# Performance work log

Hardware: AMD Instinct MI355X
Metric: run time of the kernel (lower is better)

The kernel has to match this reference:

```python
import jax, jax.numpy as jnp
import numpy as np
from jax import lax

B, H, W, CL, CC, CD, NH, NP = 8, 48, 48, 384, 384, 384, 12, 4
N = H * W
HD = CL // NH
SCALE = HD ** -0.5


def _pool_mat(n, out=7):
    # torch AdaptiveAvgPool2d bin edges: [floor(i*n/out), ceil((i+1)*n/out))
    M = np.zeros((out, n), np.float32)
    for i in range(out):
        s = (i * n) // out
        e = -(-((i + 1) * n) // out)
        M[i, s:e] = 1.0 / (e - s)
    return jnp.asarray(M)


def _resize_mat(out_n, in_n):
    # bilinear, align_corners=False (torch F.interpolate)
    M = np.zeros((out_n, in_n), np.float32)
    scale = in_n / out_n
    for o in range(out_n):
        src = (o + 0.5) * scale - 0.5
        src = min(max(src, 0.0), in_n - 1.0)
        i0 = int(np.floor(src))
        i1 = min(i0 + 1, in_n - 1)
        f = src - i0
        M[o, i0] += 1.0 - f
        M[o, i1] += f
    return jnp.asarray(M)


def _ln_c(x, g, b):
    # LayerNorm over channel dim of NCHW, eps=1e-6
    mu = jnp.mean(x, axis=1, keepdims=True)
    var = jnp.mean((x - mu) ** 2, axis=1, keepdims=True)
    xn = (x - mu) * lax.rsqrt(var + 1e-6)
    return xn * g[None, :, None, None] + b[None, :, None, None]


def _c1(x, w):
    # 1x1 conv, w: (out,in)
    return jnp.einsum('oc,bchw->bohw', w, x)


def _bilerp(feat, grid):
    # feat (G,C,Hs,Ws), grid (G,M,2) xy in [-1,1]; align_corners=False, zero padding
    G, C, Hs, Ws = feat.shape
    x = (grid[..., 0] + 1.0) * 0.5 * Ws - 0.5
    y = (grid[..., 1] + 1.0) * 0.5 * Hs - 0.5
    x0 = jnp.floor(x)
    y0 = jnp.floor(y)
    fx = x - x0
    fy = y - y0
    featf = feat.transpose(0, 2, 3, 1).reshape(G, Hs * Ws, C)
    x0i = x0.astype(jnp.int32)
    y0i = y0.astype(jnp.int32)

    def corner(ix, iy):
        valid = ((ix >= 0) & (ix < Ws) & (iy >= 0) & (iy < Hs)).astype(feat.dtype)
        flat = jnp.clip(iy, 0, Hs - 1) * Ws + jnp.clip(ix, 0, Ws - 1)
        g = jax.vmap(lambda f, i: f[i])(featf, flat)  # (G,M,C)
        return g * valid[..., None]

    v00 = corner(x0i, y0i)
    v01 = corner(x0i + 1, y0i)
    v10 = corner(x0i, y0i + 1)
    v11 = corner(x0i + 1, y0i + 1)
    w00 = ((1 - fx) * (1 - fy))[..., None]
    w01 = (fx * (1 - fy))[..., None]
    w10 = ((1 - fx) * fy)[..., None]
    w11 = (fx * fy)[..., None]
    return v00 * w00 + v01 * w01 + v10 * w10 + v11 * w11  # (G,M,C)


def _forward(local_feat, context_prior, deformable_x, W_q, W_k, W_v, W_pre, ln1_g, ln1_b,
             W_post, dw_w, dw_b, ln2_g, ln2_b, W_lo, b_lo, W_off, b_off,
             attention_biases, W_p, bn_g, bn_b, bn_mean, bn_var):
    q = _c1(local_feat, W_q)  # (B,CL,H,W)

    # context_offset_guide: 1x1 -> GELU -> adaptive pool 7x7 -> LN(C) -> 1x1 to 32 -> resize
    cg = jax.nn.gelu(_c1(context_prior, W_pre), approximate=False)
    Mh, Mw = _pool_mat(H), _pool_mat(W)
    pooled = jnp.einsum('oh,pw,bchw->bcop', Mh, Mw, cg)
    guide = _c1(_ln_c(pooled, ln1_g, ln1_b), W_post)  # (B,32,7,7)
    Uh, Uw = _resize_mat(H, 7), _resize_mat(W, 7)
    guide = jnp.einsum('Oh,Pw,bchw->bcOP', Uh, Uw, guide)  # (B,32,H,W)

    # local_offset_base: dwconv3x3 -> LN(C) -> GELU -> 1x1 to 32
    dw = lax.conv_general_dilated(local_feat, dw_w, (1, 1), [(1, 1), (1, 1)],
                                  dimension_numbers=('NCHW', 'OIHW', 'NCHW'),
                                  feature_group_count=CL) + dw_b[None, :, None, None]
    lo = jax.nn.gelu(_ln_c(dw, ln2_g, ln2_b), approximate=False)
    lo = _c1(lo, W_lo) + b_lo[None, :, None, None]  # (B,32,H,W)

    fused = jnp.concatenate([guide, lo], axis=1)  # (B,64,H,W)
    off = _c1(fused, W_off) + b_off[None, :, None, None]  # (B,NH*NP*2,H,W)
    off = off.transpose(0, 2, 3, 1).reshape(B, H, W, NH, NP, 2)
    offn = off / jnp.asarray([W, H], dtype=off.dtype)

    ry = (jnp.arange(H, dtype=off.dtype) + 0.5) / H
    rx = (jnp.arange(W, dtype=off.dtype) + 0.5) / W
    ref = jnp.stack([jnp.broadcast_to(rx[None, :], (H, W)),
                     jnp.broadcast_to(ry[:, None], (H, W))], axis=-1)  # (H,W,2) xy
    grid = (ref[None, :, :, None, None, :] + offn) * 2.0 - 1.0  # (B,H,W,NH,NP,2)

    gridh = grid.reshape(B, N, NH, NP, 2).transpose(0, 2, 1, 3, 4)  # (B,NH,N,NP,2)
    grid_r = gridh.reshape(B * NH, N * NP, 2)

    k = _c1(context_prior, W_k).reshape(B * NH, HD, H, W)
    v = _c1(deformable_x, W_v).reshape(B * NH, HD, H, W)
    k_s = _bilerp(k, grid_r).reshape(B, NH, N, NP, HD)
    v_s = _bilerp(v, grid_r).reshape(B, NH, N, NP, HD)

    qh = q.reshape(B, NH, HD, N).transpose(0, 1, 3, 2)  # (B,NH,N,HD)
    scores = jnp.einsum('bhnd,bhnpd->bhnp', qh, k_s) * SCALE

    # relative position bias: idx(p1,p2) = |dy|*W + |dx| (first-seen enumeration)
    px = jnp.clip(jnp.round((gridh[..., 0] + 1.0) * 0.5 * W - 0.5), 0, W - 1).astype(jnp.int32)
    py = jnp.clip(jnp.round((gridh[..., 1] + 1.0) * 0.5 * H - 0.5), 0, H - 1).astype(jnp.int32)
    n = jnp.arange(N, dtype=jnp.int32)
    qy = (n // W)[None, None, :, None]
    qx = (n % W)[None, None, :, None]
    bidx = jnp.abs(qy - py) * W + jnp.abs(qx - px)  # (B,NH,N,NP)
    bias = attention_biases[jnp.arange(NH)[None, :, None, None], bidx]

    attn = jax.nn.softmax(scores + bias, axis=-1)
    out = jnp.einsum('bhnp,bhnpd->bhnd', attn, v_s)  # (B,NH,N,HD)
    out = out.transpose(0, 1, 3, 2).reshape(B, CL, H, W)

    y = _c1(out, W_p)
    y = bn_g[None, :, None, None] * (y - bn_mean[None, :, None, None]) * \
        lax.rsqrt(bn_var[None, :, None, None] + 1e-5) + bn_b[None, :, None, None]
    return y


def setup_inputs():
    ks = jax.random.split(jax.random.key(0), 16)
    f32 = jnp.float32
    d = {
        'local_feat': jax.random.normal(ks[0], (B, CL, H, W), f32),
        'context_prior': jax.random.normal(ks[1], (B, CC, H, W), f32),
        'deformable_x': jax.random.normal(ks[2], (B, CD, H, W), f32),
        'W_q': jax.random.normal(ks[3], (CL, CL), f32) * 0.02,
        'W_k': jax.random.normal(ks[4], (CL, CC), f32) * 0.02,
        'W_v': jax.random.normal(ks[5], (CD, CD), f32) * 0.02,
        'W_pre': jax.random.normal(ks[6], (CC, CC), f32) * 0.02,
        'ln1_g': jnp.ones((CC,), f32),
        'ln1_b': jnp.zeros((CC,), f32),
        'W_post': jax.random.normal(ks[7], (32, CC), f32) * 0.02,
        'dw_w': jax.random.normal(ks[8], (CL, 1, 3, 3), f32) * 0.1,
        'dw_b': jnp.zeros((CL,), f32),
        'ln2_g': jnp.ones((CL,), f32),
        'ln2_b': jnp.zeros((CL,), f32),
        'W_lo': jax.random.normal(ks[9], (32, CL), f32) * 0.02,
        'b_lo': jnp.zeros((32,), f32),
        'W_off': jax.random.normal(ks[10], (NH * NP * 2, 64), f32) * 0.01,
        'b_off': jax.random.normal(ks[11], (NH * NP * 2,), f32) * 0.5,
        'attention_biases': jax.random.normal(ks[12], (NH, H * W), f32) * 0.02,
        'W_p': jax.random.normal(ks[13], (CL, CL), f32) * 0.02,
        'bn_g': jnp.ones((CL,), f32),
        'bn_b': jnp.zeros((CL,), f32),
        'bn_mean': jax.random.normal(ks[14], (CL,), f32) * 0.01,
        'bn_var': jax.random.uniform(ks[15], (CL,), f32, 0.5, 1.5),
    }
    return d


def reference(local_feat, context_prior, deformable_x, W_q, W_k, W_v, W_pre, ln1_g, ln1_b,
              W_post, dw_w, dw_b, ln2_g, ln2_b, W_lo, b_lo, W_off, b_off,
              attention_biases, W_p, bn_g, bn_b, bn_mean, bn_var):
    return _forward(local_feat, context_prior, deformable_x, W_q, W_k, W_v, W_pre, ln1_g,
                    ln1_b, W_post, dw_w, dw_b, ln2_g, ln2_b, W_lo, b_lo, W_off, b_off,
                    attention_biases, W_p, bn_g, bn_b, bn_mean, bn_var)
```

## Files before the change

### kernel.cpp

```cpp
#include <hip/hip_runtime.h>
#include <hip/hip_bf16.h>
#include <math.h>

#define B_ 8
#define H_ 48
#define W_ 48
#define N_ 2304
#define C_ 384
#define NH_ 12
#define NP_ 4
#define HD_ 32
#define SCALE_ 0.17677669529663687f

typedef unsigned short ushort;
typedef short bf16x8 __attribute__((ext_vector_type(8)));
typedef float f32x4 __attribute__((ext_vector_type(4)));

__device__ __forceinline__ float b2f(ushort u) {
    union { float f; unsigned i; } x; x.i = ((unsigned)u) << 16; return x.f;
}
__device__ __forceinline__ ushort f2b(float f) {
    __hip_bfloat16 h = __float2bfloat16(f);
    return *(ushort*)&h;
}
__device__ __forceinline__ float geluf(float x) {
    return 0.5f * x * (1.0f + erff(x * 0.70710678118654752440f));
}
__device__ __forceinline__ int iabs(int x) { return x < 0 ? -x : x; }

__device__ __forceinline__ void gl_lds16(const ushort* g, ushort* l) {
    __builtin_amdgcn_global_load_lds(
        (const __attribute__((address_space(1))) unsigned int*)g,
        (__attribute__((address_space(3))) unsigned int*)l, 16, 0, 0);
}

__global__ void probe_kernel(const void* ones_ptr, int* flag) {
    if (threadIdx.x == 0 && blockIdx.x == 0)
        *flag = (*(const unsigned*)ones_ptr == 0x3F803F80u) ? 1 : 0;
}

#define PREP_MAX 24
struct PrepTab {
    const void* src[PREP_MAX];
    void*       dst[PREP_MAX];
    int         n[PREP_MAX];
    int         tobf[PREP_MAX];
};
__global__ __launch_bounds__(256) void prep_kernel(PrepTab tab, int ne, const int* __restrict__ dflag)
{
    const int isbf = *dflag;
    const int e = blockIdx.y;
    if (e >= ne) return;
    const int n = tab.n[e];
    const void* src = tab.src[e];
    if (tab.tobf[e]) {
        ushort* dst = (ushort*)tab.dst[e];
        if (isbf) {
            const ushort* s = (const ushort*)src;
            for (int i = blockIdx.x * 256 + threadIdx.x; i < n; i += gridDim.x * 256)
                dst[i] = s[i];
        } else {
            const float* s = (const float*)src;
            for (int i = blockIdx.x * 256 + threadIdx.x; i < n; i += gridDim.x * 256)
                dst[i] = f2b(s[i]);
        }
    } else {
        float* dst = (float*)tab.dst[e];
        if (isbf) {
            const ushort* s = (const ushort*)src;
            for (int i = blockIdx.x * 256 + threadIdx.x; i < n; i += gridDim.x * 256)
                dst[i] = b2f(s[i]);
        } else {
            const float* s = (const float*)src;
            for (int i = blockIdx.x * 256 + threadIdx.x; i < n; i += gridDim.x * 256)
                dst[i] = s[i];
        }
    }
}

__global__ void dwt_prep_kernel(const float* __restrict__ WdF, float* __restrict__ WdT)
{
    int c = threadIdx.x;
#pragma unroll
    for (int u = 0; u < 9; u++) WdT[u * C_ + c] = WdF[c * 9 + u];
}

struct TPtrs { const void* src[3]; ushort* dst[3]; };
__global__ __launch_bounds__(256) void transpose3_kernel(TPtrs tp, const int* __restrict__ dflag)
{
    const int isbf = *dflag;
    const int which = blockIdx.z >> 3;
    const int b = blockIdx.z & 7;
    const int n0 = blockIdx.x * 64, c0 = blockIdx.y * 32;
    const void* in = tp.src[which];
    ushort* out = tp.dst[which];
    const int t = threadIdx.x;

    __shared__ unsigned tile[64][33];

    if (isbf) {
        {
            const int c = t >> 3, s = t & 7;
            uint4 v = *(const uint4*)((const ushort*)in + ((size_t)b * C_ + c0 + c) * N_ + n0 + s * 8);
            const int nb = s * 8;
            tile[nb + 0][c] = v.x & 0xffff; tile[nb + 1][c] = v.x >> 16;
            tile[nb + 2][c] = v.y & 0xffff; tile[nb + 3][c] = v.y >> 16;
            tile[nb + 4][c] = v.z & 0xffff; tile[nb + 5][c] = v.z >> 16;
            tile[nb + 6][c] = v.w & 0xffff; tile[nb + 7][c] = v.w >> 16;
        }
        __syncthreads();
        {
            const int n = t >> 2, s = t & 3;
            const int cb = s * 8;
            unsigned p0 = tile[n][cb + 0] | (tile[n][cb + 1] << 16);
            unsigned p1 = tile[n][cb + 2] | (tile[n][cb + 3] << 16);
            unsigned p2 = tile[n][cb + 4] | (tile[n][cb + 5] << 16);
            unsigned p3 = tile[n][cb + 6] | (tile[n][cb + 7] << 16);
            uint4 o; o.x = p0; o.y = p1; o.z = p2; o.w = p3;
            *(uint4*)(out + ((size_t)b * N_ + n0 + n) * C_ + c0 + cb) = o;
        }
    } else {
        float* tf = (float*)&tile[0][0];
        const int tx = t & 31, ty = t >> 5;
        for (int sub = 0; sub < 2; sub++) {
            int ns = n0 + sub * 32;
            __syncthreads();
#pragma unroll
            for (int u = 0; u < 4; u++) {
                int c = ty + u * 8;
                tf[c * 33 + tx] = ((const float*)in)[((size_t)b * C_ + c0 + c) * N_ + ns + tx];
            }
            __syncthreads();
#pragma unroll
            for (int u = 0; u < 4; u++) {
                int n = ty + u * 8;
                out[((size_t)b * N_ + ns + n) * C_ + c0 + tx] = f2b(tf[tx * 33 + n]);
            }
        }
    }
}

struct QKV4Ptrs { const ushort* A[4]; const ushort* Bw[4]; void* Y[4]; };
__global__ __launch_bounds__(256, 5) void gemm_qkv4_kernel(QKV4Ptrs qp)
{
    const int which = blockIdx.z >> 3;
    const int b = blockIdx.z & 7;
    const ushort* Ag = qp.A[which];
    const ushort* Bg = qp.Bw[which];

    __shared__ ushort As[2][128 * 32];
    __shared__ ushort Bs[2][128 * 32];
    const int tid = threadIdx.x;
    const int m0 = blockIdx.x * 128;
    const int n0 = blockIdx.y * 128;
    const int lane = tid & 63, wave = tid >> 6;
    const int wr = wave >> 1, wc = wave & 1;
    const int quad = lane >> 4, l15 = lane & 15;

    f32x4 acc[4][4];
#pragma unroll
    for (int i = 0; i < 4; i++)
#pragma unroll
        for (int j = 0; j < 4; j++) acc[i][j] = (f32x4){0.f, 0.f, 0.f, 0.f};

    const size_t abase = (size_t)b * (size_t)N_ * C_;

    auto stage = [&](int p, int kc) {
#pragma unroll
        for (int u = 0; u < 2; u++) {
            int idx = tid + 256 * u;
            int r = idx >> 2, s = idx & 3;
            gl_lds16(Ag + abase + (size_t)(m0 + r) * C_ + kc + 8 * s, &As[p][idx * 8]);
            gl_lds16(Bg + (size_t)(n0 + r) * C_ + kc + 8 * s, &Bs[p][idx * 8]);
        }
    };

    stage(0, 0);

    const int nt = C_ / 32;
    for (int t = 0; t < nt; ++t) {
        if (t + 1 < nt) {
            stage((t + 1) & 1, (t + 1) * 32);
            asm volatile("s_waitcnt vmcnt(4)" ::: "memory");
        } else {
            asm volatile("s_waitcnt vmcnt(0)" ::: "memory");
        }
        __builtin_amdgcn_s_barrier();
        __builtin_amdgcn_sched_barrier(0);
        const int p = t & 1;
        bf16x8 af[4], bfr[4];
#pragma unroll
        for (int i = 0; i < 4; i++)
            af[i]  = *(const bf16x8*)&As[p][(wr * 64 + i * 16 + l15) * 32 + quad * 8];
#pragma unroll
        for (int j = 0; j < 4; j++)
            bfr[j] = *(const bf16x8*)&Bs[p][(wc * 64 + j * 16 + l15) * 32 + quad * 8];
#pragma unroll
        for (int i = 0; i < 4; i++)
#pragma unroll
            for (int j = 0; j < 4; j++)
                acc[i][j] = __builtin_amdgcn_mfma_f32_16x16x32_bf16(af[i], bfr[j], acc[i][j], 0, 0, 0);
        __builtin_amdgcn_s_barrier();
    }

    if (which < 3) {
        ushort* Yg = (ushort*)qp.Y[which];
#pragma unroll
        for (int i = 0; i < 4; i++) {
#pragma unroll
            for (int r = 0; r < 4; r++) {
                int m = m0 + wr * 64 + i * 16 + quad * 4 + r;
#pragma unroll
                for (int j = 0; j < 4; j++) {
                    int nn = n0 + wc * 64 + j * 16 + l15;
                    Yg[abase + (size_t)m * C_ + nn] = f2b(acc[i][j][r]);
                }
            }
        }
    } else {
        float* Yg = (float*)qp.Y[3];
#pragma unroll
        for (int i = 0; i < 4; i++) {
#pragma unroll
            for (int r = 0; r < 4; r++) {
                int m = m0 + wr * 64 + i * 16 + quad * 4 + r;
#pragma unroll
                for (int j = 0; j < 4; j++) {
                    int nn = n0 + wc * 64 + j * 16 + l15;
                    Yg[abase + (size_t)m * C_ + nn] = geluf(acc[i][j][r]);
                }
            }
        }
    }
}

__global__ __launch_bounds__(256) void gemm_final_splitk(
    const ushort* __restrict__ WpB, const ushort* __restrict__ AOut,
    float* __restrict__ PF0, float* __restrict__ PF1)
{
    const int b  = blockIdx.z >> 1;
    const int ks = blockIdx.z & 1;
    const int kc0 = ks * 192;

    __shared__ ushort As[2][128 * 32];
    __shared__ ushort Bs[2][128 * 32];
    const int tid = threadIdx.x;
    const int m0 = blockIdx.x * 128;
    const int n0 = blockIdx.y * 128;
    const int lane = tid & 63, wave = tid >> 6;
    const int wr = wave >> 1, wc = wave & 1;
    const int quad = lane >> 4, l15 = lane & 15;

    f32x4 acc[4][4];
#pragma unroll
    for (int i = 0; i < 4; i++)
#pragma unroll
        for (int j = 0; j < 4; j++) acc[i][j] = (f32x4){0.f, 0.f, 0.f, 0.f};

    const size_t bbase = (size_t)b * (size_t)N_ * C_;

    auto stage = [&](int p, int kc) {
#pragma unroll
        for (int u = 0; u < 2; u++) {
            int idx = tid + 256 * u;
            int r = idx >> 2, s = idx & 3;
            gl_lds16(WpB + (size_t)(m0 + r) * C_ + kc0 + kc + 8 * s, &As[p][idx * 8]);
            gl_lds16(AOut + bbase + (size_t)(n0 + r) * C_ + kc0 + kc + 8 * s, &Bs[p][idx * 8]);
        }
    };

    stage(0, 0);

    const int nt = 6;
    for (int t = 0; t < nt; ++t) {
        if (t + 1 < nt) {
            stage((t + 1) & 1, (t + 1) * 32);
            asm volatile("s_waitcnt vmcnt(4)" ::: "memory");
        } else {
            asm volatile("s_waitcnt vmcnt(0)" ::: "memory");
        }
        __builtin_amdgcn_s_barrier();
        __builtin_amdgcn_sched_barrier(0);
        const int p = t & 1;
        bf16x8 af[4], bfr[4];
#pragma unroll
        for (int i = 0; i < 4; i++)
            af[i]  = *(const bf16x8*)&As[p][(wr * 64 + i * 16 + l15) * 32 + quad * 8];
#pragma unroll
        for (int j = 0; j < 4; j++)
            bfr[j] = *(const bf16x8*)&Bs[p][(wc * 64 + j * 16 + l15) * 32 + quad * 8];
#pragma unroll
        for (int i = 0; i < 4; i++)
#pragma unroll
            for (int j = 0; j < 4; j++)
                acc[i][j] = __builtin_amdgcn_mfma_f32_16x16x32_bf16(af[i], bfr[j], acc[i][j], 0, 0, 0);
        __builtin_amdgcn_s_barrier();
    }

    float* out = (ks == 0 ? PF0 : PF1) + (size_t)b * (size_t)C_ * N_;
#pragma unroll
    for (int i = 0; i < 4; i++) {
#pragma unroll
        for (int r = 0; r < 4; r++) {
            int m = m0 + wr * 64 + i * 16 + quad * 4 + r;
#pragma unroll
            for (int j = 0; j < 4; j++) {
                int nn = n0 + wc * 64 + j * 16 + l15;
                out[(size_t)m * N_ + nn] = acc[i][j][r];
            }
        }
    }
}

__global__ __launch_bounds__(256) void combine_bn_kernel(
    const float* __restrict__ PF0, const float* __restrict__ PF1,
    void* __restrict__ Yg,
    const float* __restrict__ bng, const float* __restrict__ bnb,
    const float* __restrict__ bnm, const float* __restrict__ bnv,
    const int* __restrict__ dflag)
{
    const int isbf = *dflag;
    const size_t nv4 = (size_t)B_ * C_ * N_ / 4;
    for (size_t i = blockIdx.x * 256 + threadIdx.x; i < nv4; i += (size_t)gridDim.x * 256) {
        const size_t e0 = i * 4;
        const int co = (int)((e0 / N_) % C_);
        float sc = bng[co] * rsqrtf(bnv[co] + 1e-5f);
        float sh = bnb[co] - sc * bnm[co];
        f32x4 a = *(const f32x4*)(PF0 + e0);
        f32x4 b = *(const f32x4*)(PF1 + e0);
        f32x4 v;
#pragma unroll
        for (int j = 0; j < 4; j++) v[j] = sc * (a[j] + b[j]) + sh;
        if (isbf) {
            ushort4 o;
            o.x = f2b(v[0]); o.y = f2b(v[1]); o.z = f2b(v[2]); o.w = f2b(v[3]);
            *(ushort4*)((ushort*)Yg + e0) = o;
        } else {
            *(f32x4*)((float*)Yg + e0) = v;
        }
    }
}

__global__ __launch_bounds__(384) void pool_ln_guide_kernel(
    const float* __restrict__ CG, const float* __restrict__ g, const float* __restrict__ bt,
    const ushort* __restrict__ WpostB, float* __restrict__ G7)
{
    const int cell = blockIdx.x % 49, b = blockIdx.x / 49;
    const int i = cell / 7, j = cell % 7, c = threadIdx.x;
    const int sh = (i * H_) / 7, eh = ((i + 1) * H_ + 6) / 7;
    const int sw = (j * W_) / 7, ew = ((j + 1) * W_ + 6) / 7;
    float s = 0.f;
    for (int h = sh; h < eh; h++)
        for (int w = sw; w < ew; w++)
            s += CG[((size_t)b * N_ + h * W_ + w) * C_ + c];
    s *= 1.0f / (float)((eh - sh) * (ew - sw));

    float rs = s, rq = s * s;
#pragma unroll
    for (int m = 1; m <= 32; m <<= 1) {
        rs += __shfl_xor(rs, m);
        rq += __shfl_xor(rq, m);
    }
    __shared__ float ss[6], sq[6], buf[C_];
    __shared__ float psum[12][33];
    int wid = threadIdx.x >> 6;
    if ((threadIdx.x & 63) == 0) { ss[wid] = rs; sq[wid] = rq; }
    __syncthreads();
    if (threadIdx.x == 0) {
        float ts = 0.f, tq = 0.f;
        for (int k = 0; k < 6; k++) { ts += ss[k]; tq += sq[k]; }
        ss[0] = ts; sq[0] = tq;
    }
    __syncthreads();
    float mu = ss[0] / (float)C_;
    float var = sq[0] / (float)C_ - mu * mu;
    float inv = rsqrtf(var + 1e-6f);
    buf[c] = (s - mu) * inv * g[c] + bt[c];
    __syncthreads();

    const int oc = threadIdx.x & 31, seg = threadIdx.x >> 5;
    const uint4* wp = (const uint4*)(WpostB + oc * C_ + seg * 32);
    float part = 0.f;
#pragma unroll
    for (int u = 0; u < 4; u++) {
        uint4 v = wp[u];
        const float* bb = &buf[seg * 32 + u * 8];
        part += b2f((ushort)(v.x & 0xffff)) * bb[0] + b2f((ushort)(v.x >> 16)) * bb[1];
        part += b2f((ushort)(v.y & 0xffff)) * bb[2] + b2f((ushort)(v.y >> 16)) * bb[3];
        part += b2f((ushort)(v.z & 0xffff)) * bb[4] + b2f((ushort)(v.z >> 16)) * bb[5];
        part += b2f((ushort)(v.w & 0xffff)) * bb[6] + b2f((ushort)(v.w >> 16)) * bb[7];
    }
    psum[seg][oc] = part;
    __syncthreads();
    if (threadIdx.x < 32) {
        float acc = 0.f;
#pragma unroll
        for (int k = 0; k < 12; k++) acc += psum[k][threadIdx.x];
        G7[((size_t)b * 49 + cell) * 32 + threadIdx.x] = acc;
    }
}

__global__ __launch_bounds__(384) void wcomb_prep_kernel(
    const ushort* __restrict__ WoffB, const ushort* __restrict__ WloB,
    const float* __restrict__ bloF, const float* __restrict__ boffF,
    ushort* __restrict__ Bext, float* __restrict__ biasp)
{
    const int co = blockIdx.x;
    const int c = threadIdx.x;
    float acc = 0.f;
#pragma unroll 8
    for (int j = 0; j < 32; j++)
        acc += b2f(WoffB[co * 64 + 32 + j]) * b2f(WloB[j * 384 + c]);
    ushort hi = f2b(acc);
    float r = acc - b2f(hi);
    ushort lo = f2b(r);
    Bext[co * 1152 + c] = hi;
    Bext[co * 1152 + 384 + c] = lo;
    Bext[co * 1152 + 768 + c] = hi;
    if (c == 0) {
        float bp = boffF[co];
        for (int j = 0; j < 32; j++)
            bp += b2f(WoffB[co * 64 + 32 + j]) * bloF[j];
        biasp[co] = bp;
    }
}

__global__ void og7_prep_kernel(
    const ushort* __restrict__ WoffB, const float* __restrict__ G7, float* __restrict__ OG7)
{
    const int bc = blockIdx.x;
    const int co = threadIdx.x;
    if (co >= 96) return;
    const float* g = G7 + (size_t)bc * 32;
    float acc = 0.f;
#pragma unroll 8
    for (int c = 0; c < 32; c++)
        acc += b2f(WoffB[co * 64 + c]) * g[c];
    OG7[(size_t)bc * 96 + co] = acc;
}

__global__ __launch_bounds__(512) void dw_ln_gelu_kernel(
    const ushort* __restrict__ LF, const float* __restrict__ WdT, const float* __restrict__ BdF,
    const float* __restrict__ g, const float* __restrict__ bt,
    ushort* __restrict__ AHI, ushort* __restrict__ ALO)
{
    const int wave = threadIdx.x >> 6, lane = threadIdx.x & 63;
    const int m = blockIdx.x * 8 + wave;
    const int b = m / N_, n = m % N_;
    const int h = n / W_, w = n % W_;
    const bool act = lane < 48;
    const int c0 = lane * 8;

    float acc[8];
#pragma unroll
    for (int j = 0; j < 8; j++) acc[j] = 0.f;
    if (act) {
        f32x4 b0 = *(const f32x4*)(BdF + c0);
        f32x4 b1 = *(const f32x4*)(BdF + c0 + 4);
#pragma unroll
        for (int j = 0; j < 4; j++) { acc[j] = b0[j]; acc[4 + j] = b1[j]; }
    }

#pragma unroll
    for (int u = 0; u < 9; u++) {
        const int ky = u / 3, kx = u % 3;
        const int y = h + ky - 1, x = w + kx - 1;
        if (act && y >= 0 && y < H_ && x >= 0 && x < W_) {
            uint4 v = *(const uint4*)(LF + ((size_t)b * N_ + y * W_ + x) * C_ + c0);
            f32x4 wa = *(const f32x4*)(WdT + u * C_ + c0);
            f32x4 wb = *(const f32x4*)(WdT + u * C_ + c0 + 4);
            acc[0] += wa[0] * b2f((ushort)(v.x & 0xffff));
            acc[1] += wa[1] * b2f((ushort)(v.x >> 16));
            acc[2] += wa[2] * b2f((ushort)(v.y & 0xffff));
            acc[3] += wa[3] * b2f((ushort)(v.y >> 16));
            acc[4] += wb[0] * b2f((ushort)(v.z & 0xffff));
            acc[5] += wb[1] * b2f((ushort)(v.z >> 16));
            acc[6] += wb[2] * b2f((ushort)(v.w & 0xffff));
            acc[7] += wb[3] * b2f((ushort)(v.w >> 16));
        }
    }

    float rs = 0.f, rq = 0.f;
#pragma unroll
    for (int j = 0; j < 8; j++) { rs += acc[j]; rq += acc[j] * acc[j]; }
#pragma unroll
    for (int s = 1; s <= 32; s <<= 1) {
        rs += __shfl_xor(rs, s);
        rq += __shfl_xor(rq, s);
    }
    float mu = rs / (float)C_;
    float var = rq / (float)C_ - mu * mu;
    float inv = rsqrtf(var + 1e-6f);

    if (act) {
        f32x4 g0 = *(const f32x4*)(g + c0);
        f32x4 g1 = *(const f32x4*)(g + c0 + 4);
        f32x4 t0 = *(const f32x4*)(bt + c0);
        f32x4 t1 = *(const f32x4*)(bt + c0 + 4);
        float v[8];
#pragma unroll
        for (int j = 0; j < 4; j++) {
            v[j]     = geluf((acc[j]     - mu) * inv * g0[j] + t0[j]);
            v[4 + j] = geluf((acc[4 + j] - mu) * inv * g1[j] + t1[j]);
        }
        uint4 hi, lo;
        ushort hs[8], ls[8];
#pragma unroll
        for (int j = 0; j < 8; j++) {
            hs[j] = f2b(v[j]);
            ls[j] = f2b(v[j] - b2f(hs[j]));
        }
        hi.x = (unsigned)hs[0] | ((unsigned)hs[1] << 16);
        hi.y = (unsigned)hs[2] | ((unsigned)hs[3] << 16);
        hi.z = (unsigned)hs[4] | ((unsigned)hs[5] << 16);
        hi.w = (unsigned)hs[6] | ((unsigned)hs[7] << 16);
        lo.x = (unsigned)ls[0] | ((unsigned)ls[1] << 16);
        lo.y = (unsigned)ls[2] | ((unsigned)ls[3] << 16);
        lo.z = (unsigned)ls[4] | ((unsigned)ls[5] << 16);
        lo.w = (unsigned)ls[6] | ((unsigned)ls[7] << 16);
        size_t idx = (size_t)m * C_ + c0;
        *(uint4*)(AHI + idx) = hi;
        *(uint4*)(ALO + idx) = lo;
    }
}

__global__ __launch_bounds__(256) void off_gemm_kernel(
    const ushort* __restrict__ AHI, const ushort* __restrict__ ALO,
    const ushort* __restrict__ Bext, float* __restrict__ OFFP)
{
    __shared__ ushort As[4][128 * 32];
    __shared__ ushort Bs[4][128 * 32];
    const int tid = threadIdx.x;
    const int m0 = blockIdx.x * 128;
    const int seg = blockIdx.y;
    const ushort* Ag = (seg < 2) ? AHI : ALO;
    const int bcol0 = seg * 384;
    const int lane = tid & 63, wave = tid >> 6;
    const int wr = wave >> 1, wc = wave & 1;
    const int quad = lane >> 4, l15 = lane & 15;

    f32x4 acc[4][3];
#pragma unroll
    for (int i = 0; i < 4; i++)
#pragma unroll
        for (int j = 0; j < 3; j++) acc[i][j] = (f32x4){0.f, 0.f, 0.f, 0.f};

    auto stage = [&](int p, int kc) {
#pragma unroll
        for (int u = 0; u < 2; u++) {
            int idx = tid + 256 * u;
            int r = idx >> 2, s = idx & 3;
            int rb = r < 96 ? r : 95;
            gl_lds16(Ag + (size_t)(m0 + r) * 384 + kc + 8 * s, &As[p][idx * 8]);
            gl_lds16(Bext + (size_t)rb * 1152 + bcol0 + kc + 8 * s, &Bs[p][idx * 8]);
        }
    };

    stage(0, 0);
    stage(1, 32);
    stage(2, 64);

    const int nt = 12;
    for (int t = 0; t < nt; ++t) {
        if (t + 2 < nt)      asm volatile("s_waitcnt vmcnt(8)" ::: "memory");
        else if (t + 1 < nt) asm volatile("s_waitcnt vmcnt(4)" ::: "memory");
        else                 asm volatile("s_waitcnt vmcnt(0)" ::: "memory");
        __builtin_amdgcn_s_barrier();
        __builtin_amdgcn_sched_barrier(0);
        if (t + 3 < nt) stage((t + 3) & 3, (t + 3) * 32);
        const int p = t & 3;
        bf16x8 af[4], bfr[3];
#pragma unroll
        for (int i = 0; i < 4; i++)
            af[i]  = *(const bf16x8*)&As[p][(wr * 64 + i * 16 + l15) * 32 + quad * 8];
#pragma unroll
        for (int j = 0; j < 3; j++)
            bfr[j] = *(const bf16x8*)&Bs[p][(wc * 48 + j * 16 + l15) * 32 + quad * 8];
#pragma unroll
        for (int i = 0; i < 4; i++)
#pragma unroll
            for (int j = 0; j < 3; j++)
                acc[i][j] = __builtin_amdgcn_mfma_f32_16x16x32_bf16(af[i], bfr[j], acc[i][j], 0, 0, 0);
    }

    float* out = OFFP + (size_t)seg * ((size_t)B_ * N_ * 96);
#pragma unroll
    for (int i = 0; i < 4; i++) {
#pragma unroll
        for (int r = 0; r < 4; r++) {
            int m = m0 + wr * 64 + i * 16 + quad * 4 + r;
#pragma unroll
            for (int j = 0; j < 3; j++) {
                int co = wc * 48 + j * 16 + l15;
                out[(size_t)m * 96 + co] = acc[i][j][r];
            }
        }
    }
}

__global__ __launch_bounds__(384) void attn_kernel(
    const ushort* __restrict__ Q, const ushort* __restrict__ K, const ushort* __restrict__ V,
    const float* __restrict__ OFFP, const float* __restrict__ biasp,
    const float* __restrict__ OG7,
    const float* __restrict__ ABf, ushort* __restrict__ OUT)
{
    const int pairi = blockIdx.x;
    const int b = pairi / (N_ / 2);
    const int n0 = (pairi % (N_ / 2)) * 2;
    const int tid = threadIdx.x;

    __shared__ int   cidxS[96][4];
    __shared__ float cwS[96][4];
    __shared__ float biasS[96];

    if (tid < 96) {
        const int pos = tid / 48, idx = tid % 48;
        const int n = n0 + pos;
        const int h = n / W_, w = n % W_;
        const int nh = idx >> 2, p = idx & 3;
        const int co = nh * 8 + 2 * p;

        const float fs = 7.0f / 48.0f;
        float sy = fminf(fmaxf(((float)h + 0.5f) * fs - 0.5f, 0.f), 6.f);
        float sx = fminf(fmaxf(((float)w + 0.5f) * fs - 0.5f, 0.f), 6.f);
        int gy0 = (int)floorf(sy), gx0 = (int)floorf(sx);
        int gy1 = min(gy0 + 1, 6), gx1 = min(gx0 + 1, 6);
        float gfy = sy - (float)gy0, gfx = sx - (float)gx0;
        float bw00 = (1.f - gfy) * (1.f - gfx), bw01 = (1.f - gfy) * gfx;
        float bw10 = gfy * (1.f - gfx), bw11 = gfy * gfx;
        const float* ogb = OG7 + (size_t)b * 49 * 96;
        int c00 = (gy0 * 7 + gx0) * 96, c01 = (gy0 * 7 + gx1) * 96;
        int c10 = (gy1 * 7 + gx0) * 96, c11 = (gy1 * 7 + gx1) * 96;
        const size_t MS = (size_t)B_ * N_ * 96;
        const size_t mrow = ((size_t)b * N_ + n) * 96;

        float ox = OFFP[mrow + co] + OFFP[MS + mrow + co] + OFFP[2 * MS + mrow + co]
                 + biasp[co]
                 + bw00 * ogb[c00 + co] + bw01 * ogb[c01 + co]
                 + bw10 * ogb[c10 + co] + bw11 * ogb[c11 + co];
        float oy = OFFP[mrow + co + 1] + OFFP[MS + mrow + co + 1] + OFFP[2 * MS + mrow + co + 1]
                 + biasp[co + 1]
                 + bw00 * ogb[c00 + co + 1] + bw01 * ogb[c01 + co + 1]
                 + bw10 * ogb[c10 + co + 1] + bw11 * ogb[c11 + co + 1];

        float x = (float)w + ox;
        float y = (float)h + oy;

        int px = (int)fminf(fmaxf(rintf(x), 0.f), (float)(W_ - 1));
        int py = (int)fminf(fmaxf(rintf(y), 0.f), (float)(H_ - 1));
        biasS[tid] = ABf[(size_t)nh * N_ + iabs(h - py) * W_ + iabs(w - px)];

        float x0f = floorf(x), y0f = floorf(y);
        float fx = x - x0f, fy = y - y0f;
        int x0 = (int)x0f, y0 = (int)y0f;
#pragma unroll
        for (int cc = 0; cc < 4; cc++) {
            int dx = cc & 1, dy = cc >> 1;
            int ix = x0 + dx, iy = y0 + dy;
            bool valid = (ix >= 0) && (ix < W_) && (iy >= 0) && (iy < H_);
            int ixc = min(max(ix, 0), W_ - 1), iyc = min(max(iy, 0), H_ - 1);
            cidxS[tid][cc] = iyc * W_ + ixc;
            float wx = dx ? fx : (1.f - fx);
            float wy = dy ? fy : (1.f - fy);
            cwS[tid][cc] = valid ? wx * wy : 0.f;
        }
    }
    __syncthreads();

    const int pos = tid / 192, r = tid % 192;
    const int nh = r >> 4, dd = r & 15;
    const int n = n0 + pos;
    const size_t row = ((size_t)b * N_ + n) * C_ + nh * HD_ + dd * 2;
    unsigned qu = *(const unsigned*)(Q + row);
    const float q0 = b2f((ushort)(qu & 0xffff));
    const float q1 = b2f((ushort)(qu >> 16));
    const size_t kvbase = (size_t)b * N_ * C_ + nh * HD_ + dd * 2;
    const int s0 = pos * 48 + nh * 4;

    int   ci[NP_][4];
    float cw[NP_][4];
#pragma unroll
    for (int p = 0; p < NP_; p++)
#pragma unroll
        for (int cc = 0; cc < 4; cc++) {
            ci[p][cc] = cidxS[s0 + p][cc];
            cw[p][cc] = cwS[s0 + p][cc];
        }

    float sc[NP_];
#pragma unroll
    for (int p = 0; p < NP_; p++) {
        float ks0 = 0.f, ks1 = 0.f;
#pragma unroll
        for (int cc = 0; cc < 4; cc++) {
            unsigned kv = *(const unsigned*)(K + kvbase + (size_t)ci[p][cc] * C_);
            ks0 += cw[p][cc] * b2f((ushort)(kv & 0xffff));
            ks1 += cw[p][cc] * b2f((ushort)(kv >> 16));
        }
        float dot = q0 * ks0 + q1 * ks1;
#pragma unroll
        for (int m = 1; m <= 8; m <<= 1) dot += __shfl_xor(dot, m);
        sc[p] = dot * SCALE_ + biasS[s0 + p];
    }

    float m = fmaxf(fmaxf(sc[0], sc[1]), fmaxf(sc[2], sc[3]));
    float e[NP_], esum = 0.f;
#pragma unroll
    for (int p = 0; p < NP_; p++) { e[p] = __expf(sc[p] - m); esum += e[p]; }
    float inv = 1.0f / esum;

    float o0 = 0.f, o1 = 0.f;
#pragma unroll
    for (int p = 0; p < NP_; p++) {
        float vs0 = 0.f, vs1 = 0.f;
#pragma unroll
        for (int cc = 0; cc < 4; cc++) {
            unsigned vv = *(const unsigned*)(V + kvbase + (size_t)ci[p][cc] * C_);
            vs0 += cw[p][cc] * b2f((ushort)(vv & 0xffff));
            vs1 += cw[p][cc] * b2f((ushort)(vv >> 16));
        }
        float ep = e[p] * inv;
        o0 += ep * vs0;
        o1 += ep * vs1;
    }
    unsigned ou = (unsigned)f2b(o0) | ((unsigned)f2b(o1) << 16);
    *(unsigned*)(OUT + row) = ou;
}

extern "C" void kernel_launch(void* const* d_in, const int* in_sizes, int n_in,
                              void* d_out, int out_size, void* d_ws, size_t ws_size,
                              hipStream_t stream)
{
    const void* local_feat    = d_in[0];
    const void* context_prior = d_in[1];
    const void* deformable_x  = d_in[2];

    const size_t BIGE = (size_t)B_ * N_ * C_;

    char* wsb = (char*)d_ws;
    auto carve = [&](size_t bytes) { char* p = wsb; wsb += (bytes + 255) & ~(size_t)255; return p; };
    int*    flag = (int*)carve(256);
    ushort* T1   = (ushort*)carve(BIGE * 2);
    ushort* T2   = (ushort*)carve(BIGE * 2);
    ushort* T3   = (ushort*)carve(BIGE * 2);
    ushort* Qb   = (ushort*)carve(BIGE * 2);
    ushort* Kb   = (ushort*)carve(BIGE * 2);
    ushort* Vb   = (ushort*)carve(BIGE * 2);
    ushort* AHI  = (ushort*)carve(BIGE * 2);
    ushort* ALO  = (ushort*)carve(BIGE * 2);
    float*  CGR  = (float*)carve(BIGE * 4);
    float*  OFFB = (float*)carve((size_t)B_ * N_ * 96 * 4 * 3);
    float*  G7   = (float*)carve((size_t)B_ * 49 * 32 * 4);
    ushort* WqB   = (ushort*)carve(147456 * 2);
    ushort* WkB   = (ushort*)carve(147456 * 2);
    ushort* WvB   = (ushort*)carve(147456 * 2);
    ushort* WpreB = (ushort*)carve(147456 * 2);
    ushort* WpB   = (ushort*)carve(147456 * 2);
    ushort* WpostB= (ushort*)carve(12288 * 2);
    ushort* WloB  = (ushort*)carve(12288 * 2);
    ushort* WoffB = (ushort*)carve(6144 * 2);
    ushort* Bext  = (ushort*)carve(96 * 1152 * 2);
    float*  biasp = (float*)carve(96 * 4);
    float*  OG7   = (float*)carve((size_t)B_ * 49 * 96 * 4);
    float*  dwwF  = (float*)carve(3456 * 4);
    float*  dwwT  = (float*)carve(3456 * 4);
    float*  ABf   = (float*)carve(27648 * 4);
    float*  bloF  = (float*)carve(32 * 4);
    float*  boffF = (float*)carve(96 * 4);
    float*  dwbF  = (float*)carve(384 * 4);
    float*  ln1gF = (float*)carve(384 * 4);
    float*  ln1bF = (float*)carve(384 * 4);
    float*  ln2gF = (float*)carve(384 * 4);
    float*  ln2bF = (float*)carve(384 * 4);
    float*  bngF  = (float*)carve(384 * 4);
    float*  bnbF  = (float*)carve(384 * 4);
    float*  bnmF  = (float*)carve(384 * 4);
    float*  bnvF  = (float*)carve(384 * 4);
    ushort* AOut = (ushort*)CGR + BIGE;
    float*  PF0  = (float*)T1;
    float*  PF1  = (float*)T3;

    probe_kernel<<<1, 64, 0, stream>>>(d_in[7] , flag);

    PrepTab tab;
    int ne = 0;
    auto add = [&](const void* s, void* d, int n, int tb) {
        tab.src[ne] = s; tab.dst[ne] = d; tab.n[ne] = n; tab.tobf[ne] = tb; ne++;
    };
    add(d_in[3],  WqB,   147456, 1);
    add(d_in[4],  WkB,   147456, 1);
    add(d_in[5],  WvB,   147456, 1);
    add(d_in[6],  WpreB, 147456, 1);
    add(d_in[19], WpB,   147456, 1);
    add(d_in[9],  WpostB, 12288, 1);
    add(d_in[14], WloB,   12288, 1);
    add(d_in[16], WoffB,   6144, 1);
    add(d_in[10], dwwF,    3456, 0);
    add(d_in[18], ABf,    27648, 0);
    add(d_in[15], bloF,      32, 0);
    add(d_in[17], boffF,     96, 0);
    add(d_in[11], dwbF,     384, 0);
    add(d_in[7],  ln1gF,    384, 0);
    add(d_in[8],  ln1bF,    384, 0);
    add(d_in[12], ln2gF,    384, 0);
    add(d_in[13], ln2bF,    384, 0);
    add(d_in[20], bngF,     384, 0);
    add(d_in[21], bnbF,     384, 0);
    add(d_in[22], bnmF,     384, 0);
    add(d_in[23], bnvF,     384, 0);
    prep_kernel<<<dim3(64, ne), 256, 0, stream>>>(tab, ne, flag);
    dwt_prep_kernel<<<1, 384, 0, stream>>>(dwwF, dwwT);

    dim3 blk256(256);
    dim3 t3grid(N_ / 64, C_ / 32, 3 * B_);
    dim3 qkv4grid(N_ / 128, C_ / 128, 4 * B_);
    dim3 offgrid((B_ * N_) / 128, 3);
    dim3 fingrid(C_ / 128, N_ / 128, 2 * B_);

    TPtrs tp;
    tp.src[0] = local_feat;    tp.dst[0] = T1;
    tp.src[1] = context_prior; tp.dst[1] = T2;
    tp.src[2] = deformable_x;  tp.dst[2] = T3;
    transpose3_kernel<<<t3grid, blk256, 0, stream>>>(tp, flag);

    wcomb_prep_kernel<<<96, 384, 0, stream>>>(WoffB, WloB, bloF, boffF, Bext, biasp);

    dw_ln_gelu_kernel<<<(B_ * N_) / 8, 512, 0, stream>>>(T1, dwwT, dwbF, ln2gF, ln2bF, AHI, ALO);

    off_gemm_kernel<<<offgrid, blk256, 0, stream>>>(AHI, ALO, Bext, OFFB);

    QKV4Ptrs qp;
    qp.A[0] = T1; qp.Bw[0] = WqB;   qp.Y[0] = Qb;
    qp.A[1] = T2; qp.Bw[1] = WkB;   qp.Y[1] = Kb;
    qp.A[2] = T3; qp.Bw[2] = WvB;   qp.Y[2] = Vb;
    qp.A[3] = T2; qp.Bw[3] = WpreB; qp.Y[3] = CGR;
    gemm_qkv4_kernel<<<qkv4grid, blk256, 0, stream>>>(qp);

    pool_ln_guide_kernel<<<B_ * 49, 384, 0, stream>>>(CGR, ln1gF, ln1bF, WpostB, G7);
    og7_prep_kernel<<<B_ * 49, 96, 0, stream>>>(WoffB, G7, OG7);

    attn_kernel<<<(B_ * N_) / 2, 384, 0, stream>>>(Qb, Kb, Vb, OFFB, biasp, OG7, ABf, AOut);

    gemm_final_splitk<<<fingrid, blk256, 0, stream>>>(WpB, AOut, PF0, PF1);

    combine_bn_kernel<<<2048, blk256, 0, stream>>>(PF0, PF1, d_out, bngF, bnbF, bnmF, bnvF, flag);
}
```

Before: 357.1 us.

## Fuse BN into final GEMM, swizzle LDS tiles, remap block order for XCD locality

The split-K final projection GEMM and the separate combine/BatchNorm kernel are replaced by one full-K GEMM with 128x64 tiles that applies BN and writes the output directly. This removes the fp32 partial-sum round trip through memory and one launch. All three MFMA GEMMs now XOR-swizzle the 16-byte chunks in LDS to cut bank conflicts. The QKV and final GEMMs use a 1D grid with a block-index remap that spreads contiguous work across the 8 XCDs, aiming at better L2 locality. The fused epilogue writes elements one at a time with a dtype branch, which may coalesce worse than the old vectorised combine.

```diff
diff --git a/kernel.cpp b/kernel.cpp
--- a/kernel.cpp
+++ b/kernel.cpp
@@ -143,19 +143,21 @@
 struct QKV4Ptrs { const ushort* A[4]; const ushort* Bw[4]; void* Y[4]; };
 __global__ __launch_bounds__(256, 5) void gemm_qkv4_kernel(QKV4Ptrs qp)
 {
-    const int which = blockIdx.z >> 3;
-    const int b = blockIdx.z & 7;
+    const int l = (blockIdx.x & 7) * 216 + (blockIdx.x >> 3);
+    const int zc = l / 54, r2 = l % 54;
+    const int which = zc >> 3, b = zc & 7;
+    const int m0 = (r2 / 3) * 128;
+    const int n0 = (r2 % 3) * 128;
     const ushort* Ag = qp.A[which];
     const ushort* Bg = qp.Bw[which];
 
     __shared__ ushort As[2][128 * 32];
     __shared__ ushort Bs[2][128 * 32];
     const int tid = threadIdx.x;
-    const int m0 = blockIdx.x * 128;
-    const int n0 = blockIdx.y * 128;
     const int lane = tid & 63, wave = tid >> 6;
     const int wr = wave >> 1, wc = wave & 1;
     const int quad = lane >> 4, l15 = lane & 15;
+    const int sx = (quad ^ (l15 & 3)) * 8;
 
     f32x4 acc[4][4];
 #pragma unroll
@@ -169,9 +171,10 @@
 #pragma unroll
         for (int u = 0; u < 2; u++) {
             int idx = tid + 256 * u;
-            int r = idx >> 2, s = idx & 3;
-            gl_lds16(Ag + abase + (size_t)(m0 + r) * C_ + kc + 8 * s, &As[p][idx * 8]);
-            gl_lds16(Bg + (size_t)(n0 + r) * C_ + kc + 8 * s, &Bs[p][idx * 8]);
+            int r = idx >> 2, sl = idx & 3;
+            int sg = sl ^ (r & 3);
+            gl_lds16(Ag + abase + (size_t)(m0 + r) * C_ + kc + 8 * sg, &As[p][idx * 8]);
+            gl_lds16(Bg + (size_t)(n0 + r) * C_ + kc + 8 * sg, &Bs[p][idx * 8]);
         }
     };
 
@@ -191,10 +194,10 @@
         bf16x8 af[4], bfr[4];
 #pragma unroll
         for (int i = 0; i < 4; i++)
-            af[i]  = *(const bf16x8*)&As[p][(wr * 64 + i * 16 + l15) * 32 + quad * 8];
+            af[i]  = *(const bf16x8*)&As[p][(wr * 64 + i * 16 + l15) * 32 + sx];
 #pragma unroll
         for (int j = 0; j < 4; j++)
-            bfr[j] = *(const bf16x8*)&Bs[p][(wc * 64 + j * 16 + l15) * 32 + quad * 8];
+            bfr[j] = *(const bf16x8*)&Bs[p][(wc * 64 + j * 16 + l15) * 32 + sx];
 #pragma unroll
         for (int i = 0; i < 4; i++)
 #pragma unroll
@@ -234,109 +237,93 @@
     }
 }
 
-__global__ __launch_bounds__(256) void gemm_final_splitk(
+__global__ __launch_bounds__(256) void gemm_final_kernel(
     const ushort* __restrict__ WpB, const ushort* __restrict__ AOut,
-    float* __restrict__ PF0, float* __restrict__ PF1)
-{
-    const int b  = blockIdx.z >> 1;
-    const int ks = blockIdx.z & 1;
-    const int kc0 = ks * 192;
-
-    __shared__ ushort As[2][128 * 32];
-    __shared__ ushort Bs[2][128 * 32];
-    const int tid = threadIdx.x;
-    const int m0 = blockIdx.x * 128;
-    const int n0 = blockIdx.y * 128;
-    const int lane = tid & 63, wave = tid >> 6;
-    const int wr = wave >> 1, wc = wave & 1;
-    const int quad = lane >> 4, l15 = lane & 15;
-
-    f32x4 acc[4][4];
-#pragma unroll
-    for (int i = 0; i < 4; i++)
-#pragma unroll
-        for (int j = 0; j < 4; j++) acc[i][j] = (f32x4){0.f, 0.f, 0.f, 0.f};
-
-    const size_t bbase = (size_t)b * (size_t)N_ * C_;
-
-    auto stage = [&](int p, int kc) {
-#pragma unroll
-        for (int u = 0; u < 2; u++) {
-            int idx = tid + 256 * u;
-            int r = idx >> 2, s = idx & 3;
-            gl_lds16(WpB + (size_t)(m0 + r) * C_ + kc0 + kc + 8 * s, &As[p][idx * 8]);
-            gl_lds16(AOut + bbase + (size_t)(n0 + r) * C_ + kc0 + kc + 8 * s, &Bs[p][idx * 8]);
-        }
-    };
-
-    stage(0, 0);
-
-    const int nt = 6;
-    for (int t = 0; t < nt; ++t) {
-        if (t + 1 < nt) {
-            stage((t + 1) & 1, (t + 1) * 32);
-            asm volatile("s_waitcnt vmcnt(4)" ::: "memory");
-        } else {
-            asm volatile("s_waitcnt vmcnt(0)" ::: "memory");
-        }
-        __builtin_amdgcn_s_barrier();
-        __builtin_amdgcn_sched_barrier(0);
-        const int p = t & 1;
-        bf16x8 af[4], bfr[4];
-#pragma unroll
-        for (int i = 0; i < 4; i++)
-            af[i]  = *(const bf16x8*)&As[p][(wr * 64 + i * 16 + l15) * 32 + quad * 8];
-#pragma unroll
-        for (int j = 0; j < 4; j++)
-            bfr[j] = *(const bf16x8*)&Bs[p][(wc * 64 + j * 16 + l15) * 32 + quad * 8];
-#pragma unroll
-        for (int i = 0; i < 4; i++)
-#pragma unroll
-            for (int j = 0; j < 4; j++)
-                acc[i][j] = __builtin_amdgcn_mfma_f32_16x16x32_bf16(af[i], bfr[j], acc[i][j], 0, 0, 0);
-        __builtin_amdgcn_s_barrier();
-    }
-
-    float* out = (ks == 0 ? PF0 : PF1) + (size_t)b * (size_t)C_ * N_;
-#pragma unroll
-    for (int i = 0; i < 4; i++) {
-#pragma unroll
-        for (int r = 0; r < 4; r++) {
-            int m = m0 + wr * 64 + i * 16 + quad * 4 + r;
-#pragma unroll
-            for (int j = 0; j < 4; j++) {
-                int nn = n0 + wc * 64 + j * 16 + l15;
-                out[(size_t)m * N_ + nn] = acc[i][j][r];
-            }
-        }
-    }
-}
-
-__global__ __launch_bounds__(256) void combine_bn_kernel(
-    const float* __restrict__ PF0, const float* __restrict__ PF1,
     void* __restrict__ Yg,
     const float* __restrict__ bng, const float* __restrict__ bnb,
     const float* __restrict__ bnm, const float* __restrict__ bnv,
     const int* __restrict__ dflag)
 {
     const int isbf = *dflag;
-    const size_t nv4 = (size_t)B_ * C_ * N_ / 4;
-    for (size_t i = blockIdx.x * 256 + threadIdx.x; i < nv4; i += (size_t)gridDim.x * 256) {
-        const size_t e0 = i * 4;
-        const int co = (int)((e0 / N_) % C_);
-        float sc = bng[co] * rsqrtf(bnv[co] + 1e-5f);
-        float sh = bnb[co] - sc * bnm[co];
-        f32x4 a = *(const f32x4*)(PF0 + e0);
-        f32x4 b = *(const f32x4*)(PF1 + e0);
-        f32x4 v;
-#pragma unroll
-        for (int j = 0; j < 4; j++) v[j] = sc * (a[j] + b[j]) + sh;
-        if (isbf) {
-            ushort4 o;
-            o.x = f2b(v[0]); o.y = f2b(v[1]); o.z = f2b(v[2]); o.w = f2b(v[3]);
-            *(ushort4*)((ushort*)Yg + e0) = o;
+    const int l = (blockIdx.x & 7) * 108 + (blockIdx.x >> 3);
+    const int b = l / 108, r2 = l % 108;
+    const int n0 = (r2 / 3) * 64;
+    const int m0 = (r2 % 3) * 128;
+
+    __shared__ ushort As[2][128 * 32];
+    __shared__ ushort Bs[2][64 * 32];
+    const int tid = threadIdx.x;
+    const int lane = tid & 63, wave = tid >> 6;
+    const int quad = lane >> 4, l15 = lane & 15;
+    const int sx = (quad ^ (l15 & 3)) * 8;
+
+    f32x4 acc[2][4];
+#pragma unroll
+    for (int i = 0; i < 2; i++)
+#pragma unroll
+        for (int j = 0; j < 4; j++) acc[i][j] = (f32x4){0.f, 0.f, 0.f, 0.f};
+
+    const size_t bbase = (size_t)b * (size_t)N_ * C_;
+
+    auto stage = [&](int p, int kc) {
+#pragma unroll
+        for (int u = 0; u < 2; u++) {
+            int idx = tid + 256 * u;
+            int r = idx >> 2, sl = idx & 3;
+            int sg = sl ^ (r & 3);
+            gl_lds16(WpB + (size_t)(m0 + r) * C_ + kc + 8 * sg, &As[p][idx * 8]);
+        }
+        {
+            int r = tid >> 2, sl = tid & 3;
+            int sg = sl ^ (r & 3);
+            gl_lds16(AOut + bbase + (size_t)(n0 + r) * C_ + kc + 8 * sg, &Bs[p][tid * 8]);
+        }
+    };
+
+    stage(0, 0);
+
+    const int nt = C_ / 32;
+    for (int t = 0; t < nt; ++t) {
+        if (t + 1 < nt) {
+            stage((t + 1) & 1, (t + 1) * 32);
+            asm volatile("s_waitcnt vmcnt(3)" ::: "memory");
         } else {
-            *(f32x4*)((float*)Yg + e0) = v;
+            asm volatile("s_waitcnt vmcnt(0)" ::: "memory");
+        }
+        __builtin_amdgcn_s_barrier();
+        __builtin_amdgcn_sched_barrier(0);
+        const int p = t & 1;
+        bf16x8 af[2], bfr[4];
+#pragma unroll
+        for (int i = 0; i < 2; i++)
+            af[i]  = *(const bf16x8*)&As[p][(wave * 32 + i * 16 + l15) * 32 + sx];
+#pragma unroll
+        for (int j = 0; j < 4; j++)
+            bfr[j] = *(const bf16x8*)&Bs[p][(j * 16 + l15) * 32 + sx];
+#pragma unroll
+        for (int i = 0; i < 2; i++)
+#pragma unroll
+            for (int j = 0; j < 4; j++)
+                acc[i][j] = __builtin_amdgcn_mfma_f32_16x16x32_bf16(af[i], bfr[j], acc[i][j], 0, 0, 0);
+        __builtin_amdgcn_s_barrier();
+    }
+
+    const size_t ybase = (size_t)b * (size_t)C_ * N_;
+#pragma unroll
+    for (int i = 0; i < 2; i++) {
+#pragma unroll
+        for (int r = 0; r < 4; r++) {
+            int m = m0 + wave * 32 + i * 16 + quad * 4 + r;
+            float sc = bng[m] * rsqrtf(bnv[m] + 1e-5f);
+            float sh = bnb[m] - sc * bnm[m];
+#pragma unroll
+            for (int j = 0; j < 4; j++) {
+                int nn = n0 + j * 16 + l15;
+                float v = sc * acc[i][j][r] + sh;
+                size_t yi = ybase + (size_t)m * N_ + nn;
+                if (isbf) ((ushort*)Yg)[yi] = f2b(v);
+                else ((float*)Yg)[yi] = v;
+            }
         }
     }
 }
@@ -538,6 +525,7 @@
     const int lane = tid & 63, wave = tid >> 6;
     const int wr = wave >> 1, wc = wave & 1;
     const int quad = lane >> 4, l15 = lane & 15;
+    const int sx = (quad ^ (l15 & 3)) * 8;
 
     f32x4 acc[4][3];
 #pragma unroll
@@ -549,10 +537,11 @@
 #pragma unroll
         for (int u = 0; u < 2; u++) {
             int idx = tid + 256 * u;
-            int r = idx >> 2, s = idx & 3;
+            int r = idx >> 2, sl = idx & 3;
+            int sg = sl ^ (r & 3);
             int rb = r < 96 ? r : 95;
-            gl_lds16(Ag + (size_t)(m0 + r) * 384 + kc + 8 * s, &As[p][idx * 8]);
-            gl_lds16(Bext + (size_t)rb * 1152 + bcol0 + kc + 8 * s, &Bs[p][idx * 8]);
+            gl_lds16(Ag + (size_t)(m0 + r) * 384 + kc + 8 * sg, &As[p][idx * 8]);
+            gl_lds16(Bext + (size_t)rb * 1152 + bcol0 + kc + 8 * sg, &Bs[p][idx * 8]);
         }
     };
 
@@ -572,10 +561,10 @@
         bf16x8 af[4], bfr[3];
 #pragma unroll
         for (int i = 0; i < 4; i++)
-            af[i]  = *(const bf16x8*)&As[p][(wr * 64 + i * 16 + l15) * 32 + quad * 8];
+            af[i]  = *(const bf16x8*)&As[p][(wr * 64 + i * 16 + l15) * 32 + sx];
 #pragma unroll
         for (int j = 0; j < 3; j++)
-            bfr[j] = *(const bf16x8*)&Bs[p][(wc * 48 + j * 16 + l15) * 32 + quad * 8];
+            bfr[j] = *(const bf16x8*)&Bs[p][(wc * 48 + j * 16 + l15) * 32 + sx];
 #pragma unroll
         for (int i = 0; i < 4; i++)
 #pragma unroll
@@ -777,8 +766,6 @@
     float*  bnmF  = (float*)carve(384 * 4);
     float*  bnvF  = (float*)carve(384 * 4);
     ushort* AOut = (ushort*)CGR + BIGE;
-    float*  PF0  = (float*)T1;
-    float*  PF1  = (float*)T3;
 
     probe_kernel<<<1, 64, 0, stream>>>(d_in[7] , flag);
 
@@ -813,9 +800,7 @@
 
     dim3 blk256(256);
     dim3 t3grid(N_ / 64, C_ / 32, 3 * B_);
-    dim3 qkv4grid(N_ / 128, C_ / 128, 4 * B_);
     dim3 offgrid((B_ * N_) / 128, 3);
-    dim3 fingrid(C_ / 128, N_ / 128, 2 * B_);
 
     TPtrs tp;
     tp.src[0] = local_feat;    tp.dst[0] = T1;
@@ -834,14 +819,13 @@
     qp.A[1] = T2; qp.Bw[1] = WkB;   qp.Y[1] = Kb;
     qp.A[2] = T3; qp.Bw[2] = WvB;   qp.Y[2] = Vb;
     qp.A[3] = T2; qp.Bw[3] = WpreB; qp.Y[3] = CGR;
-    gemm_qkv4_kernel<<<qkv4grid, blk256, 0, stream>>>(qp);
+    gemm_qkv4_kernel<<<1728, blk256, 0, stream>>>(qp);
 
     pool_ln_guide_kernel<<<B_ * 49, 384, 0, stream>>>(CGR, ln1gF, ln1bF, WpostB, G7);
     og7_prep_kernel<<<B_ * 49, 96, 0, stream>>>(WoffB, G7, OG7);
 
     attn_kernel<<<(B_ * N_) / 2, 384, 0, stream>>>(Qb, Kb, Vb, OFFB, biasp, OG7, ABf, AOut);
 
-    gemm_final_splitk<<<fingrid, blk256, 0, stream>>>(WpB, AOut, PF0, PF1);
-
-    combine_bn_kernel<<<2048, blk256, 0, stream>>>(PF0, PF1, d_out, bngF, bnbF, bnmF, bnvF, flag);
-}
+    gemm_final_kernel<<<864, blk256, 0, stream>>>(
+        WpB, AOut, d_out, bngF, bnbF, bnmF, bnvF, flag);
+}
```

Result: faster. 346.4 us (-3.0%).
